# Optimization experiments

Hardware: AMD Instinct MI355X
Metric: run time of the kernel (lower is better)

## Reference

```python
import jax, jax.numpy as jnp
import numpy as np

N = 50000        # nodes
E = 1_600_000    # edges
F_IN = 128
HID = 128
OUT = 128
NEG_SLOPE = 0.2  # PyG GATConv default


def _gat_layer(x, src, dst, W, a_src, a_dst, b, n_nodes):
    """PyG GATConv (heads=1, add_self_loops handled by caller)."""
    h = x @ W                                   # [N, d_out]
    alpha_src = h @ a_src                       # [N]
    alpha_dst = h @ a_dst                       # [N]
    e = jax.nn.leaky_relu(alpha_src[src] + alpha_dst[dst], NEG_SLOPE)  # [E']
    # segment softmax over incoming edges of each destination node
    m = jax.ops.segment_max(e, dst, num_segments=n_nodes)
    e = jnp.exp(e - m[dst])
    s = jax.ops.segment_sum(e, dst, num_segments=n_nodes)
    alpha = e / s[dst]                          # [E']
    out = jax.ops.segment_sum(alpha[:, None] * h[src], dst, num_segments=n_nodes)
    return out + b


def setup_inputs() -> dict:
    key = jax.random.key(0)
    ks = jax.random.split(key, 11)
    sW1 = 1.0 / np.sqrt(F_IN)
    sW2 = 1.0 / np.sqrt(HID)
    return {
        "x": jax.random.normal(ks[0], (N, F_IN), dtype=jnp.float32),
        "edge_index": jax.random.randint(ks[1], (2, E), 0, N, dtype=jnp.int64
                                         if jax.config.jax_enable_x64 else jnp.int32),
        "W1": jax.random.normal(ks[2], (F_IN, HID), dtype=jnp.float32) * sW1,
        "a1_src": jax.random.normal(ks[3], (HID,), dtype=jnp.float32) * sW2,
        "a1_dst": jax.random.normal(ks[4], (HID,), dtype=jnp.float32) * sW2,
        "b1": jnp.zeros((HID,), dtype=jnp.float32),
        "W2": jax.random.normal(ks[5], (HID, OUT), dtype=jnp.float32) * sW2,
        "a2_src": jax.random.normal(ks[6], (OUT,), dtype=jnp.float32) * sW2,
        "a2_dst": jax.random.normal(ks[7], (OUT,), dtype=jnp.float32) * sW2,
        "b2": jnp.zeros((OUT,), dtype=jnp.float32),
    }


def reference(x, edge_index, W1, a1_src, a1_dst, b1, W2, a2_src, a2_dst, b2):
    n = x.shape[0]
    loop = jnp.arange(n, dtype=edge_index.dtype)
    src = jnp.concatenate([edge_index[0], loop])   # add self loops (PyG default)
    dst = jnp.concatenate([edge_index[1], loop])
    h = _gat_layer(x, src, dst, W1, a1_src, a1_dst, b1, n)
    h = jax.nn.relu(h)
    # F.dropout with training=False is identity (eval-mode reference)
    out = _gat_layer(h, src, dst, W2, a2_src, a2_dst, b2, n)
    return out
```

## Files before the change

### kernel.cpp

```cpp
#include <hip/hip_runtime.h>
#include <hip/hip_bf16.h>
#include <hip/hip_fp16.h>

#define FD 128
#define CBW 64
#define NB_MAX 1024

typedef _Float16 half8 __attribute__((ext_vector_type(8)));
typedef float f32x4 __attribute__((ext_vector_type(4)));

__global__ __launch_bounds__(256) void k_chist(const int* __restrict__ dst,
                                               int* __restrict__ ccnt, int e, int nb) {
    __shared__ int lh[NB_MAX];
    for (int i = threadIdx.x; i < nb; i += 256) lh[i] = 0;
    __syncthreads();
    for (int i = blockIdx.x * 256 + threadIdx.x; i < e; i += gridDim.x * 256)
        atomicAdd(&lh[dst[i] >> 6], 1);
    __syncthreads();
    for (int i = threadIdx.x; i < nb; i += 256) {
        int c = lh[i];
        if (c) atomicAdd(&ccnt[i], c);
    }
}

__global__ void k_cscan(const int* __restrict__ ccnt, int* __restrict__ cbase,
                        int* __restrict__ ccur, int nb, int* __restrict__ rowptr, int n) {
    __shared__ int wsum[16];
    __shared__ int woff[17];
    const int t = threadIdx.x, lane = t & 63, wid = t >> 6;
    int carry = 0;
    for (int base = 0; base < nb; base += 1024) {
        int idx = base + t;
        int v = (idx < nb) ? ccnt[idx] : 0;
        int s = v;
#pragma unroll
        for (int off = 1; off < 64; off <<= 1) {
            int u = __shfl_up(s, off, 64);
            if (lane >= off) s += u;
        }
        if (lane == 63) wsum[wid] = s;
        __syncthreads();
        if (wid == 0) {
            int w2 = (lane < 16) ? wsum[lane] : 0;
#pragma unroll
            for (int off = 1; off < 16; off <<= 1) {
                int u = __shfl_up(w2, off, 64);
                if (lane >= off) w2 += u;
            }
            if (lane < 16) woff[lane + 1] = w2;
            if (lane == 0) woff[0] = 0;
        }
        __syncthreads();
        int excl = carry + woff[wid] + (s - v);
        if (idx < nb) { cbase[idx] = excl; ccur[idx] = excl; }
        carry += woff[16];
        __syncthreads();
    }
    if (t == 0) { cbase[nb] = carry; rowptr[n] = carry; }
}

__global__ __launch_bounds__(256) void k_cscatter(const int* __restrict__ src,
                                                  const int* __restrict__ dst,
                                                  int* __restrict__ ccur,
                                                  int* __restrict__ ebuf,
                                                  int e, int nb, int nblocks) {
    __shared__ int lh[NB_MAX];
    __shared__ int lb[NB_MAX];
    const int per = (e + nblocks - 1) / nblocks;
    const int lo = blockIdx.x * per;
    const int hi = min(e, lo + per);
    const int t = threadIdx.x;
    for (int i = t; i < nb; i += 256) lh[i] = 0;
    __syncthreads();
    for (int i = lo + t; i < hi; i += 256) atomicAdd(&lh[dst[i] >> 6], 1);
    __syncthreads();
    for (int i = t; i < nb; i += 256) {
        int c = lh[i];
        lb[i] = c ? atomicAdd(&ccur[i], c) : 0;
    }
    __syncthreads();
    for (int i = t; i < nb; i += 256) lh[i] = 0;
    __syncthreads();
    for (int i = lo + t; i < hi; i += 256) {
        int d = dst[i];
        int bkt = d >> 6;
        int r = atomicAdd(&lh[bkt], 1);
        ebuf[lb[bkt] + r] = (src[i] << 6) | (d & (CBW - 1));
    }
}

__global__ __launch_bounds__(256) void k_fine(const int* __restrict__ ebuf,
                                              const int* __restrict__ cbase,
                                              int* __restrict__ rowptr,
                                              int* __restrict__ colidx, int n) {
    const int b = blockIdx.x;
    const int node0 = b * CBW;
    const int nloc = min(CBW, n - node0);
    const int beg = cbase[b], end = cbase[b + 1];
    __shared__ int fh[CBW];
    __shared__ int fo[CBW];
    const int t = threadIdx.x;
    if (t < CBW) fh[t] = 0;
    __syncthreads();
    for (int e = beg + t; e < end; e += 256) atomicAdd(&fh[ebuf[e] & (CBW - 1)], 1);
    __syncthreads();
    if (t < 64) {
        int v = fh[t];
        int s = v;
#pragma unroll
        for (int off = 1; off < 64; off <<= 1) {
            int u = __shfl_up(s, off, 64);
            if (t >= off) s += u;
        }
        fo[t] = s - v;
    }
    __syncthreads();
    if (t < nloc) rowptr[node0 + t] = beg + fo[t];
    if (t < CBW) fh[t] = 0;
    __syncthreads();
    for (int e = beg + t; e < end; e += 256) {
        int v = ebuf[e];
        int d = v & (CBW - 1);
        int r = atomicAdd(&fh[d], 1);
        colidx[beg + fo[d] + r] = v >> 6;
    }
}

__global__ __launch_bounds__(1024) void k_wt(const float* __restrict__ Wa,
                                             const float* __restrict__ Wb,
                                             __half* __restrict__ Ta,
                                             __half* __restrict__ Tb) {
    __shared__ float sw[128 * 129];
    const float* W = blockIdx.x ? Wb : Wa;
    __half* T = blockIdx.x ? Tb : Ta;
    const int t = threadIdx.x;
#pragma unroll
    for (int i = 0; i < 16; i++) {
        int idx = i * 1024 + t;
        sw[(idx >> 7) * 129 + (idx & 127)] = W[idx];
    }
    __syncthreads();
#pragma unroll
    for (int i = 0; i < 8; i++) {
        int o = i * 1024 + t;
        int c = o >> 6, kp = o & 63;
        float lo = sw[(kp * 2) * 129 + c];
        float hi = sw[(kp * 2 + 1) * 129 + c];
        *(__half2*)&T[c * 128 + kp * 2] = __floats2half2_rn(lo, hi);
    }
}

__global__ __launch_bounds__(256) void k_x16(const float* __restrict__ x,
                                             __half* __restrict__ y, int count8) {
    int i = blockIdx.x * 256 + threadIdx.x;
    if (i >= count8) return;
    float4 a = *(const float4*)&x[(size_t)i * 8];
    float4 b = *(const float4*)&x[(size_t)i * 8 + 4];
    union { __half2 h2[4]; uint4 u; } pk;
    pk.h2[0] = __floats2half2_rn(a.x, a.y);
    pk.h2[1] = __floats2half2_rn(a.z, a.w);
    pk.h2[2] = __floats2half2_rn(b.x, b.y);
    pk.h2[3] = __floats2half2_rn(b.z, b.w);
    *(uint4*)&y[(size_t)i * 8] = pk.u;
}

__global__ __launch_bounds__(256) void k_gemm(const __half* __restrict__ X,
                                              const __half* __restrict__ Wt,
                                              const float* __restrict__ a_s,
                                              const float* __restrict__ a_d,
                                              __half* __restrict__ H,
                                              float* __restrict__ as_,
                                              float* __restrict__ ad_, int n) {
    const int t = threadIdx.x;
    const int wave = t >> 6, lane = t & 63;
    const int g = lane >> 4, c16 = lane & 15;
    const int row0 = blockIdx.x * 64 + wave * 16;

    half8 A[4];
    {
        int row = row0 + c16;
        int rc = (row < n) ? row : (n - 1);
        const __half* xp = &X[(size_t)rc * 128 + g * 8];
#pragma unroll
        for (int kc = 0; kc < 4; kc++) A[kc] = *(const half8*)(xp + kc * 32);
    }

    f32x4 acc[8];
#pragma unroll
    for (int ct = 0; ct < 8; ct++) acc[ct] = (f32x4){0.f, 0.f, 0.f, 0.f};

#pragma unroll
    for (int ct = 0; ct < 8; ct++) {
        const __half* wp = &Wt[(ct * 16 + c16) * 128 + g * 8];
#pragma unroll
        for (int kc = 0; kc < 4; kc++) {
            half8 b = *(const half8*)(wp + kc * 32);
            acc[ct] = __builtin_amdgcn_mfma_f32_16x16x32_f16(A[kc], b, acc[ct], 0, 0, 0);
        }
    }

    float asv[8], adv[8];
#pragma unroll
    for (int ct = 0; ct < 8; ct++) {
        asv[ct] = a_s[ct * 16 + c16];
        adv[ct] = a_d[ct * 16 + c16];
    }
#pragma unroll
    for (int r = 0; r < 4; r++) {
        const int row = row0 + g * 4 + r;
        float vs = 0.f, vd = 0.f;
#pragma unroll
        for (int ct = 0; ct < 8; ct++) {
            float v = acc[ct][r];
            vs += v * asv[ct];
            vd += v * adv[ct];
            if (row < n) H[(size_t)row * 128 + ct * 16 + c16] = __float2half(v);
        }
#pragma unroll
        for (int off = 8; off; off >>= 1) {
            vs += __shfl_xor(vs, off, 16);
            vd += __shfl_xor(vd, off, 16);
        }
        if (c16 == 0 && row < n) { as_[row] = vs; ad_[row] = vd; }
    }
}

__device__ __forceinline__ void fmix8(float* acc, uint4 hv, float w) {
    union { uint4 u; _Float16 h[8]; } c;
    c.u = hv;
#pragma unroll
    for (int j = 0; j < 8; j++) acc[j] += w * (float)c.h[j];
}

__global__ __launch_bounds__(256) void k_aggr(const __half* __restrict__ H,
                                              const float* __restrict__ as_,
                                              const float* __restrict__ ad_,
                                              const int* __restrict__ rowptr,
                                              const int* __restrict__ colidx,
                                              const float* __restrict__ bias,
                                              float* __restrict__ outf,
                                              __half* __restrict__ outh,
                                              int n, int mode) {
    const int wid = threadIdx.x >> 6;
    const int lane = threadIdx.x & 63;
    const int node = blockIdx.x * 4 + wid;
    if (node >= n) return;
    const int q = lane >> 4;
    const int l = lane & 15;
    const int f0 = l * 8;
    const float adn = ad_[node];
    float s_acc = 0.f;
    float acc[8] = {0.f, 0.f, 0.f, 0.f, 0.f, 0.f, 0.f, 0.f};
    const int beg = rowptr[node], end = rowptr[node + 1];

    if (q == 3) {
        float e = as_[node] + adn;
        e = (e > 0.f) ? e : 0.2f * e;
        const float w = __expf(e);
        s_acc += w;
        fmix8(acc, *(const uint4*)&H[(size_t)node * 128 + f0], w);
    }

    int it = beg;
    int s[4]; float a[4];
#pragma unroll
    for (int j = 0; j < 4; j++) {
        int idx = it + q + 4 * j;
        s[j] = node; a[j] = -1e30f;
        if (idx < end) { s[j] = colidx[idx]; a[j] = as_[s[j]]; }
    }
    while (it < end) {
        uint4 h[4]; float w[4];
#pragma unroll
        for (int j = 0; j < 4; j++) {
            int idx = it + q + 4 * j;
            h[j] = make_uint4(0u, 0u, 0u, 0u);
            if (idx < end) h[j] = *(const uint4*)&H[(size_t)s[j] * 128 + f0];
        }
#pragma unroll
        for (int j = 0; j < 4; j++) {
            float e = a[j] + adn;
            e = (e > 0.f) ? e : 0.2f * e;
            w[j] = __expf(e);
        }
        const int nit = it + 16;
        int ns[4]; float na[4];
#pragma unroll
        for (int j = 0; j < 4; j++) {
            int idx = nit + q + 4 * j;
            ns[j] = node; na[j] = -1e30f;
            if (idx < end) { ns[j] = colidx[idx]; na[j] = as_[ns[j]]; }
        }
#pragma unroll
        for (int j = 0; j < 4; j++) { s_acc += w[j]; fmix8(acc, h[j], w[j]); }
#pragma unroll
        for (int j = 0; j < 4; j++) { s[j] = ns[j]; a[j] = na[j]; }
        it = nit;
    }

#pragma unroll
    for (int off = 16; off <= 32; off <<= 1) {
        s_acc += __shfl_xor(s_acc, off);
#pragma unroll
        for (int j = 0; j < 8; j++) acc[j] += __shfl_xor(acc[j], off);
    }
    if (q == 0) {
        const float inv = 1.f / s_acc;
        float o[8];
        const float4 b0 = *(const float4*)&bias[f0];
        const float4 b1 = *(const float4*)&bias[f0 + 4];
        o[0] = acc[0] * inv + b0.x; o[1] = acc[1] * inv + b0.y;
        o[2] = acc[2] * inv + b0.z; o[3] = acc[3] * inv + b0.w;
        o[4] = acc[4] * inv + b1.x; o[5] = acc[5] * inv + b1.y;
        o[6] = acc[6] * inv + b1.z; o[7] = acc[7] * inv + b1.w;
        if (mode == 1) {
#pragma unroll
            for (int j = 0; j < 8; j++) o[j] = fmaxf(o[j], 0.f);
            union { __half2 h2[4]; uint4 u; } pk;
            pk.h2[0] = __floats2half2_rn(o[0], o[1]);
            pk.h2[1] = __floats2half2_rn(o[2], o[3]);
            pk.h2[2] = __floats2half2_rn(o[4], o[5]);
            pk.h2[3] = __floats2half2_rn(o[6], o[7]);
            *(uint4*)&outh[(size_t)node * 128 + f0] = pk.u;
        } else {
            *(float4*)&outf[(size_t)node * 128 + f0] = make_float4(o[0], o[1], o[2], o[3]);
            *(float4*)&outf[(size_t)node * 128 + f0 + 4] = make_float4(o[4], o[5], o[6], o[7]);
        }
    }
}

extern "C" void kernel_launch(void* const* d_in, const int* in_sizes, int n_in,
                              void* d_out, int out_size, void* d_ws, size_t ws_size,
                              hipStream_t stream) {
    const float* x   = (const float*)d_in[0];
    const int*   ei  = (const int*)d_in[1];
    const float* W1  = (const float*)d_in[2];
    const float* a1s = (const float*)d_in[3];
    const float* a1d = (const float*)d_in[4];
    const float* b1  = (const float*)d_in[5];
    const float* W2  = (const float*)d_in[6];
    const float* a2s = (const float*)d_in[7];
    const float* a2d = (const float*)d_in[8];
    const float* b2  = (const float*)d_in[9];
    float* dout = (float*)d_out;

    const int n = in_sizes[0] / FD;
    const int E = in_sizes[1] / 2;
    const int* src = ei;
    const int* dst = ei + E;
    const int NB = (n + CBW - 1) / CBW;

    char* base = (char*)d_ws;
    __half* buf0  = (__half*)base;
    int*    ebuf  = (int*)base;
    __half* H     = (__half*)(base + (size_t)n * FD * sizeof(__half));
    float* as_    = (float*)((char*)H + (size_t)n * FD * sizeof(__half));
    float* ad_    = as_ + n;
    int*   rowptr = (int*)(ad_ + n);
    int*   ccnt   = rowptr + (n + 1);
    int*   cbase  = ccnt + NB;
    int*   ccur   = cbase + NB + 1;
    int*   colidx = ccur + NB;
    size_t wt_off = (((size_t)((char*)(colidx + E) - base)) + 15) & ~(size_t)15;
    __half* Wt1h  = (__half*)(base + wt_off);
    __half* Wt2h  = Wt1h + 128 * 128;

    k_wt<<<2, 1024, 0, stream>>>(W1, W2, Wt1h, Wt2h);
    hipMemsetAsync(ccnt, 0, (size_t)NB * sizeof(int), stream);
    k_chist<<<256, 256, 0, stream>>>(dst, ccnt, E, NB);
    k_cscan<<<1, 1024, 0, stream>>>(ccnt, cbase, ccur, NB, rowptr, n);
    const int SCAT_BLOCKS = 256;
    k_cscatter<<<SCAT_BLOCKS, 256, 0, stream>>>(src, dst, ccur, ebuf, E, NB, SCAT_BLOCKS);
    k_fine<<<NB, 256, 0, stream>>>(ebuf, cbase, rowptr, colidx, n);

    const int count8 = n * FD / 8;
    k_x16<<<(count8 + 255) / 256, 256, 0, stream>>>(x, buf0, count8);

    const int gemm_grid = (n + 63) / 64;
    const int node_grid = (n + 3) / 4;

    k_gemm<<<gemm_grid, 256, 0, stream>>>(buf0, Wt1h, a1s, a1d, H, as_, ad_, n);
    k_aggr<<<node_grid, 256, 0, stream>>>(H, as_, ad_, rowptr, colidx, b1,
                                          nullptr, buf0, n, 1);

    k_gemm<<<gemm_grid, 256, 0, stream>>>(buf0, Wt2h, a2s, a2d, H, as_, ad_, n);
    k_aggr<<<node_grid, 256, 0, stream>>>(H, as_, ad_, rowptr, colidx, b2,
                                          dout, nullptr, n, 0);
}
```

Baseline: 245.1 us.

## Restructure edge aggregation with wave-wide coalesced index loads and merge prep kernels

The aggregation kernel now has each wave load up to 64 edge indices and attention logits at once, one per lane, compute all edge weights in parallel, and broadcast source ids and weights by shuffle to the 16-lane feature groups. This replaces the per-quarter 4-edge software pipeline and its dependent colidx→as_ loads, cutting the latency chain per edge. Self-loop weight handling and softmax denominator reduction move to a full-wave xor reduce. The weight transpose and the x-to-fp16 conversion kernels are fused into one launch to save a kernel launch. The fused prep kernel uses 1024-thread blocks for the conversion part and reserves a large shared-memory array in every block, which may lower occupancy.

New measurement: 237.9 us. -2.9%, faster.

```diff
diff --git a/kernel.cpp b/kernel.cpp
--- a/kernel.cpp
+++ b/kernel.cpp
@@ -126,42 +126,43 @@
     }
 }
 
-__global__ __launch_bounds__(1024) void k_wt(const float* __restrict__ Wa,
-                                             const float* __restrict__ Wb,
-                                             __half* __restrict__ Ta,
-                                             __half* __restrict__ Tb) {
-    __shared__ float sw[128 * 129];
-    const float* W = blockIdx.x ? Wb : Wa;
-    __half* T = blockIdx.x ? Tb : Ta;
+__global__ __launch_bounds__(1024) void k_prep(const float* __restrict__ W1,
+                                               const float* __restrict__ W2,
+                                               __half* __restrict__ T1,
+                                               __half* __restrict__ T2,
+                                               const float* __restrict__ x,
+                                               __half* __restrict__ x16, int count8) {
     const int t = threadIdx.x;
-#pragma unroll
-    for (int i = 0; i < 16; i++) {
-        int idx = i * 1024 + t;
-        sw[(idx >> 7) * 129 + (idx & 127)] = W[idx];
-    }
-    __syncthreads();
-#pragma unroll
-    for (int i = 0; i < 8; i++) {
-        int o = i * 1024 + t;
-        int c = o >> 6, kp = o & 63;
-        float lo = sw[(kp * 2) * 129 + c];
-        float hi = sw[(kp * 2 + 1) * 129 + c];
-        *(__half2*)&T[c * 128 + kp * 2] = __floats2half2_rn(lo, hi);
-    }
-}
-
-__global__ __launch_bounds__(256) void k_x16(const float* __restrict__ x,
-                                             __half* __restrict__ y, int count8) {
-    int i = blockIdx.x * 256 + threadIdx.x;
-    if (i >= count8) return;
-    float4 a = *(const float4*)&x[(size_t)i * 8];
-    float4 b = *(const float4*)&x[(size_t)i * 8 + 4];
-    union { __half2 h2[4]; uint4 u; } pk;
-    pk.h2[0] = __floats2half2_rn(a.x, a.y);
-    pk.h2[1] = __floats2half2_rn(a.z, a.w);
-    pk.h2[2] = __floats2half2_rn(b.x, b.y);
-    pk.h2[3] = __floats2half2_rn(b.z, b.w);
-    *(uint4*)&y[(size_t)i * 8] = pk.u;
+    if (blockIdx.x < 2) {
+        __shared__ float sw[128 * 129];
+        const float* W = blockIdx.x ? W2 : W1;
+        __half* T = blockIdx.x ? T2 : T1;
+#pragma unroll
+        for (int i = 0; i < 16; i++) {
+            int idx = i * 1024 + t;
+            sw[(idx >> 7) * 129 + (idx & 127)] = W[idx];
+        }
+        __syncthreads();
+#pragma unroll
+        for (int i = 0; i < 8; i++) {
+            int o = i * 1024 + t;
+            int c = o >> 6, kp = o & 63;
+            float lo = sw[(kp * 2) * 129 + c];
+            float hi = sw[(kp * 2 + 1) * 129 + c];
+            *(__half2*)&T[c * 128 + kp * 2] = __floats2half2_rn(lo, hi);
+        }
+    } else {
+        int i = (blockIdx.x - 2) * 1024 + t;
+        if (i >= count8) return;
+        float4 a = *(const float4*)&x[(size_t)i * 8];
+        float4 b = *(const float4*)&x[(size_t)i * 8 + 4];
+        union { __half2 h2[4]; uint4 u; } pk;
+        pk.h2[0] = __floats2half2_rn(a.x, a.y);
+        pk.h2[1] = __floats2half2_rn(a.z, a.w);
+        pk.h2[2] = __floats2half2_rn(b.x, b.y);
+        pk.h2[3] = __floats2half2_rn(b.z, b.w);
+        *(uint4*)&x16[(size_t)i * 8] = pk.u;
+    }
 }
 
 __global__ __launch_bounds__(256) void k_gemm(const __half* __restrict__ X,
@@ -246,66 +247,55 @@
     const int node = blockIdx.x * 4 + wid;
     if (node >= n) return;
     const int q = lane >> 4;
-    const int l = lane & 15;
-    const int f0 = l * 8;
+    const int boff = (lane & 15) * 16;
     const float adn = ad_[node];
-    float s_acc = 0.f;
+    float sp = 0.f;
     float acc[8] = {0.f, 0.f, 0.f, 0.f, 0.f, 0.f, 0.f, 0.f};
     const int beg = rowptr[node], end = rowptr[node + 1];
 
-    if (q == 3) {
+    {
         float e = as_[node] + adn;
         e = (e > 0.f) ? e : 0.2f * e;
         const float w = __expf(e);
-        s_acc += w;
-        fmix8(acc, *(const uint4*)&H[(size_t)node * 128 + f0], w);
-    }
-
-    int it = beg;
-    int s[4]; float a[4];
-#pragma unroll
-    for (int j = 0; j < 4; j++) {
-        int idx = it + q + 4 * j;
-        s[j] = node; a[j] = -1e30f;
-        if (idx < end) { s[j] = colidx[idx]; a[j] = as_[s[j]]; }
-    }
-    while (it < end) {
-        uint4 h[4]; float w[4];
-#pragma unroll
-        for (int j = 0; j < 4; j++) {
-            int idx = it + q + 4 * j;
-            h[j] = make_uint4(0u, 0u, 0u, 0u);
-            if (idx < end) h[j] = *(const uint4*)&H[(size_t)s[j] * 128 + f0];
-        }
-#pragma unroll
-        for (int j = 0; j < 4; j++) {
-            float e = a[j] + adn;
-            e = (e > 0.f) ? e : 0.2f * e;
-            w[j] = __expf(e);
-        }
-        const int nit = it + 16;
-        int ns[4]; float na[4];
-#pragma unroll
-        for (int j = 0; j < 4; j++) {
-            int idx = nit + q + 4 * j;
-            ns[j] = node; na[j] = -1e30f;
-            if (idx < end) { ns[j] = colidx[idx]; na[j] = as_[ns[j]]; }
-        }
-#pragma unroll
-        for (int j = 0; j < 4; j++) { s_acc += w[j]; fmix8(acc, h[j], w[j]); }
-#pragma unroll
-        for (int j = 0; j < 4; j++) { s[j] = ns[j]; a[j] = na[j]; }
-        it = nit;
-    }
-
+        if (lane == 63) sp += w;
+        if (q == 3) {
+            const uint4 hv = *(const uint4*)((const char*)H + (((unsigned)node << 8) + boff));
+            fmix8(acc, hv, w);
+        }
+    }
+
+    for (int it = beg; it < end; it += 64) {
+        const int idx = it + lane;
+        const bool valid = idx < end;
+        const int idxc = valid ? idx : (end - 1);
+        const int sl = colidx[idxc];
+        float e = as_[sl] + adn;
+        e = (e > 0.f) ? e : 0.2f * e;
+        const float w = valid ? __expf(e) : 0.f;
+        sp += w;
+        int m = end - it; if (m > 64) m = 64;
+        const int iters = (m + 3) >> 2;
+        int slot = q;
+#pragma unroll 4
+        for (int g = 0; g < iters; ++g) {
+            const int srcg = __shfl(sl, slot, 64);
+            const float wg = __shfl(w, slot, 64);
+            const uint4 hv = *(const uint4*)((const char*)H + (((unsigned)srcg << 8) + boff));
+            fmix8(acc, hv, wg);
+            slot += 4;
+        }
+    }
+
+#pragma unroll
+    for (int off = 1; off < 64; off <<= 1) sp += __shfl_xor(sp, off);
 #pragma unroll
     for (int off = 16; off <= 32; off <<= 1) {
-        s_acc += __shfl_xor(s_acc, off);
 #pragma unroll
         for (int j = 0; j < 8; j++) acc[j] += __shfl_xor(acc[j], off);
     }
     if (q == 0) {
-        const float inv = 1.f / s_acc;
+        const int f0 = boff >> 1;
+        const float inv = 1.f / sp;
         float o[8];
         const float4 b0 = *(const float4*)&bias[f0];
         const float4 b1 = *(const float4*)&bias[f0 + 4];
@@ -365,7 +355,6 @@
     __half* Wt1h  = (__half*)(base + wt_off);
     __half* Wt2h  = Wt1h + 128 * 128;
 
-    k_wt<<<2, 1024, 0, stream>>>(W1, W2, Wt1h, Wt2h);
     hipMemsetAsync(ccnt, 0, (size_t)NB * sizeof(int), stream);
     k_chist<<<256, 256, 0, stream>>>(dst, ccnt, E, NB);
     k_cscan<<<1, 1024, 0, stream>>>(ccnt, cbase, ccur, NB, rowptr, n);
@@ -374,7 +363,8 @@
     k_fine<<<NB, 256, 0, stream>>>(ebuf, cbase, rowptr, colidx, n);
 
     const int count8 = n * FD / 8;
-    k_x16<<<(count8 + 255) / 256, 256, 0, stream>>>(x, buf0, count8);
+    const int prep_grid = 2 + (count8 + 1023) / 1024;
+    k_prep<<<prep_grid, 1024, 0, stream>>>(W1, W2, Wt1h, Wt2h, x, buf0, count8);
 
     const int gemm_grid = (n + 63) / 64;
     const int node_grid = (n + 3) / 4;
```
